# Kernel tuning notes

Hardware: AMD Instinct MI355X
Metric: run time of the kernel (lower is better)

Reference implementation:

```python
import jax, jax.numpy as jnp
import numpy as np

C_TOTAL = 201      # n_classes + 1 (background)
N_CLASSES = 200
K = 5              # n_prototypes
DIM = 768
GAMMA = 0.999
TEMPERATURE = 0.2
THRESH = 0.8       # assignment_threshold


def l2norm(x, axis=-1, eps=1e-12):
    return x / jnp.maximum(jnp.linalg.norm(x, axis=axis, keepdims=True), eps)


def setup_inputs() -> dict:
    key = jax.random.key(0)
    k0, k1, k2, k3, k4 = jax.random.split(key, 5)
    B, H, W = 32, 32, 32
    N = H * W
    patch_tokens = jax.random.normal(k0, (B, N, DIM), jnp.float32)
    raw_patch_tokens = jax.random.normal(k1, (B, N, DIM), jnp.float32)
    # trunc_normal_(std=0.02) init of the prototype buffer
    prototypes = jax.random.truncated_normal(k2, -2.0, 2.0, (C_TOTAL, K, DIM), jnp.float32) * 0.02
    sa_weights = jnp.ones((N_CLASSES, K), jnp.float32)  # constant init -> uniform softmax, same as 0.5
    labels = jax.random.randint(k3, (32,), 0, N_CLASSES)
    sam_masks = jax.random.randint(k4, (B, H, W), 0, 2, dtype=jnp.int32)
    return {
        'patch_tokens': patch_tokens,
        'raw_patch_tokens': raw_patch_tokens,
        'prototypes': prototypes,
        'sa_weights': sa_weights,
        'labels': labels,
        'sam_masks': sam_masks,
    }


def reference(patch_tokens, raw_patch_tokens, prototypes, sa_weights, labels, sam_masks):
    B, N, D = patch_tokens.shape
    H = W = int(np.sqrt(N))

    # --- prototype matching ---
    pt = l2norm(patch_tokens)
    proto_n = l2norm(prototypes)
    # [B, N, C, K] cosine logits
    logits = jnp.einsum('bnd,ckd->bnck', pt, proto_n)
    image_prototype_logits = logits.max(axis=1)                    # [B, C, K]
    saw = jax.nn.softmax(sa_weights, axis=-1) * K                  # ScoreAggregation
    class_logits = (image_prototype_logits[:, :-1, :] * saw).sum(-1) / TEMPERATURE  # [B, n_classes]

    # --- pseudo patch labels (sam_masks already at (H, W) -> nearest interp is identity) ---
    pm = sam_masks.astype(jnp.float32)                             # [B, H, W]
    pseudo = jnp.where(pm == 1.0, labels[:, None, None], N_CLASSES)  # [B, H, W] int

    # --- online clustering (vectorized over the per-class python loop) ---
    raw = l2norm(raw_patch_tokens).reshape(B * N, D)               # detached in original
    lab_flat = pseudo.reshape(-1)                                  # [BN]
    L = logits.reshape(B * N, C_TOTAL, K)
    # gather each token's logits for its own (pseudo) class: L[n, lab_flat[n], :]
    Lc = jnp.take_along_axis(L, lab_flat[:, None, None], axis=1)[:, 0, :]  # [BN, K]
    A = jax.nn.softmax(Lc, axis=-1)
    max_vals = A.max(axis=-1)
    indices = A.argmax(axis=-1)
    # threshold then L1-renormalize (zero rows stay zero, matching F.normalize eps)
    A = jnp.where(max_vals[:, None] < THRESH, 0.0, A)
    A = A / jnp.maximum(A.sum(axis=-1, keepdims=True), 1e-12)
    # per-class soft-kmeans centroid accumulation: P_c_new = A_c^T @ I_c
    wx = A[:, :, None] * raw[:, None, :]                           # [BN, K, D]
    P_c_new = jax.ops.segment_sum(wx, lab_flat, num_segments=C_TOTAL)  # [C, K, D]
    counts = jax.ops.segment_sum(jnp.ones_like(lab_flat), lab_flat, num_segments=C_TOTAL)
    present = (counts > 0)[:, None, None]
    # momentum EMA update, only for classes present in the batch
    P_new = jnp.where(present, GAMMA * prototypes + (1.0 - GAMMA) * P_c_new, prototypes)

    part_assignment_maps = (indices + lab_flat * K).reshape(B, H * W)

    return (class_logits, image_prototype_logits, logits, part_assignment_maps, P_new, pseudo)
```

## Files before the change

kernel.cpp:

```cpp
#include <hip/hip_runtime.h>
#include <math.h>

#define Bv   32
#define Nv   1024
#define Dv   768
#define Cv   201
#define Kv   5
#define CKv  1005
#define BNv  32768
#define NCLS 200

#define OFF_CL     0
#define OFF_IPL    6400
#define OFF_LOG    38560
#define OFF_PART   32970400
#define OFF_PNEW   33003168
#define OFF_PSEUDO 33775008

typedef short bf16x8 __attribute__((ext_vector_type(8)));
typedef float f32x4  __attribute__((ext_vector_type(4)));
typedef float f32x4u __attribute__((ext_vector_type(4), aligned(4)));
typedef __attribute__((address_space(1))) const unsigned int g_u32;
typedef __attribute__((address_space(3))) unsigned int l_u32;

__device__ inline unsigned short f2bf(float f) {
  unsigned u = __float_as_uint(f);
  u += 0x7fffu + ((u >> 16) & 1u);
  return (unsigned short)(u >> 16);
}
__device__ inline unsigned fenc(float f) {
  unsigned u = __float_as_uint(f);
  return u ^ (((unsigned)((int)u >> 31)) | 0x80000000u);
}
__device__ inline float fdec(unsigned u) {
  unsigned bits = (u & 0x80000000u) ? (u ^ 0x80000000u) : ~u;
  return __uint_as_float(bits);
}

__global__ __launch_bounds__(256) void prep_kernel(
    const float* __restrict__ pt, const float* __restrict__ raw,
    const float* __restrict__ proto,
    unsigned short* __restrict__ Ah, unsigned short* __restrict__ Bh,
    float* __restrict__ inv_raw, int* __restrict__ zbuf, int zn, int ZB) {
  if ((int)blockIdx.x < ZB) {
    int i = blockIdx.x * 256 + threadIdx.x;
    if (i < zn) zbuf[i] = 0;
    return;
  }
  const int rbase = (blockIdx.x - ZB) * 16 + (threadIdx.x >> 6) * 4;
  const int l = threadIdx.x & 63;

  if (rbase < BNv) {
    const float* src = pt + (size_t)rbase * Dv;
    float4 v[4][3];
#pragma unroll
    for (int r = 0; r < 4; ++r)
#pragma unroll
      for (int i = 0; i < 3; ++i)
        v[r][i] = reinterpret_cast<const float4*>(src + (size_t)r * Dv)[i * 64 + l];
    float s[4];
#pragma unroll
    for (int r = 0; r < 4; ++r)
      s[r] = v[r][0].x * v[r][0].x + v[r][0].y * v[r][0].y + v[r][0].z * v[r][0].z + v[r][0].w * v[r][0].w
           + v[r][1].x * v[r][1].x + v[r][1].y * v[r][1].y + v[r][1].z * v[r][1].z + v[r][1].w * v[r][1].w
           + v[r][2].x * v[r][2].x + v[r][2].y * v[r][2].y + v[r][2].z * v[r][2].z + v[r][2].w * v[r][2].w;
#pragma unroll
    for (int off = 32; off > 0; off >>= 1)
#pragma unroll
      for (int r = 0; r < 4; ++r) s[r] += __shfl_xor(s[r], off);
#pragma unroll
    for (int r = 0; r < 4; ++r) {
      float inv = 1.0f / fmaxf(sqrtf(s[r]), 1e-12f);
      unsigned short* dst = Ah + (size_t)(rbase + r) * Dv;
#pragma unroll
      for (int i = 0; i < 3; ++i) {
        float a0 = v[r][i].x * inv, a1 = v[r][i].y * inv;
        float a2 = v[r][i].z * inv, a3 = v[r][i].w * inv;
        *reinterpret_cast<ushort4*>(dst + i * 256 + 4 * l) =
            make_ushort4(f2bf(a0), f2bf(a1), f2bf(a2), f2bf(a3));
      }
    }
    return;
  }
  if (rbase < BNv + 1024) {
    const int rp0 = rbase - BNv;
    float4 v[4][3];
#pragma unroll
    for (int r = 0; r < 4; ++r) {
      int rp = rp0 + r;
      int rs = (rp < CKv) ? rp : (CKv - 1);
      const float* src = proto + (size_t)rs * Dv;
#pragma unroll
      for (int i = 0; i < 3; ++i)
        v[r][i] = reinterpret_cast<const float4*>(src)[i * 64 + l];
    }
    float s[4];
#pragma unroll
    for (int r = 0; r < 4; ++r)
      s[r] = v[r][0].x * v[r][0].x + v[r][0].y * v[r][0].y + v[r][0].z * v[r][0].z + v[r][0].w * v[r][0].w
           + v[r][1].x * v[r][1].x + v[r][1].y * v[r][1].y + v[r][1].z * v[r][1].z + v[r][1].w * v[r][1].w
           + v[r][2].x * v[r][2].x + v[r][2].y * v[r][2].y + v[r][2].z * v[r][2].z + v[r][2].w * v[r][2].w;
#pragma unroll
    for (int off = 32; off > 0; off >>= 1)
#pragma unroll
      for (int r = 0; r < 4; ++r) s[r] += __shfl_xor(s[r], off);
#pragma unroll
    for (int r = 0; r < 4; ++r) {
      int rp = rp0 + r;
      unsigned short* dst = Bh + (size_t)rp * Dv;
      float inv = (rp < CKv) ? 1.0f / fmaxf(sqrtf(s[r]), 1e-12f) : 0.0f;
#pragma unroll
      for (int i = 0; i < 3; ++i) {
        float a0 = v[r][i].x * inv, a1 = v[r][i].y * inv;
        float a2 = v[r][i].z * inv, a3 = v[r][i].w * inv;
        ushort4 w = (rp < CKv)
            ? make_ushort4(f2bf(a0), f2bf(a1), f2bf(a2), f2bf(a3))
            : make_ushort4(0, 0, 0, 0);
        *reinterpret_cast<ushort4*>(dst + i * 256 + 4 * l) = w;
      }
    }
    return;
  }
  if (rbase < 2 * BNv + 1024) {
    const int rr = rbase - BNv - 1024;
    const float* src = raw + (size_t)rr * Dv;
    float s[4];
#pragma unroll
    for (int r = 0; r < 4; ++r) {
      float4 v0 = reinterpret_cast<const float4*>(src + (size_t)r * Dv)[l];
      float4 v1 = reinterpret_cast<const float4*>(src + (size_t)r * Dv)[64 + l];
      float4 v2 = reinterpret_cast<const float4*>(src + (size_t)r * Dv)[128 + l];
      s[r] = v0.x * v0.x + v0.y * v0.y + v0.z * v0.z + v0.w * v0.w
           + v1.x * v1.x + v1.y * v1.y + v1.z * v1.z + v1.w * v1.w
           + v2.x * v2.x + v2.y * v2.y + v2.z * v2.z + v2.w * v2.w;
    }
#pragma unroll
    for (int off = 32; off > 0; off >>= 1)
#pragma unroll
      for (int r = 0; r < 4; ++r) s[r] += __shfl_xor(s[r], off);
    if (l == 0) {
#pragma unroll
      for (int r = 0; r < 4; ++r)
        inv_raw[rr + r] = 1.0f / fmaxf(sqrtf(s[r]), 1e-12f);
    }
  }
}

#define BM 256
#define BN 128
__global__ __launch_bounds__(512) void gemm_mfma_kernel(
    const unsigned short* __restrict__ Ah, const unsigned short* __restrict__ Bh,
    float* __restrict__ Co, unsigned int* __restrict__ iplU) {
  __shared__ __align__(16) unsigned char smem[49152];
#define LA(b) ((unsigned short (*)[32])(smem + (b) * 16384))
#define LB(b) ((unsigned short (*)[32])(smem + 32768 + (b) * 8192))
  const int tid  = threadIdx.x;
  const int wid  = tid >> 6;
  const int lane = tid & 63;
  const int wm = wid >> 1, wn = wid & 1;
  const int orig = blockIdx.x;
  const int wgid = ((orig & 7) << 7) | (orig >> 3);
  const int m0 = (wgid >> 3) * BM, n0 = (wgid & 7) * BN;
  const int fr = lane & 15;
  const int q  = lane >> 4;

  f32x4 acc[4][4];
#pragma unroll
  for (int i = 0; i < 4; ++i)
#pragma unroll
    for (int j = 0; j < 4; ++j)
#pragma unroll
      for (int r = 0; r < 4; ++r) acc[i][j][r] = 0.f;

  const int ra = wid * 16 + (lane >> 2);
  const int sa = (lane & 3) ^ ((ra >> 1) & 3);
  const unsigned short* srcA0 = Ah + (size_t)(m0 + ra) * Dv + sa * 8;
  const unsigned short* srcA1 = Ah + (size_t)(m0 + 128 + ra) * Dv + sa * 8;
  const unsigned short* srcB0 = Bh + (size_t)(n0 + ra) * Dv + sa * 8;

#define STG_A0(buf, t) __builtin_amdgcn_global_load_lds((g_u32*)(srcA0 + (t) * 32), \
    (l_u32*)&LA(buf)[wid * 16][0], 16, 0, 0)
#define STG_A1(buf, t) __builtin_amdgcn_global_load_lds((g_u32*)(srcA1 + (t) * 32), \
    (l_u32*)&LA(buf)[128 + wid * 16][0], 16, 0, 0)
#define STG_B0(buf, t) __builtin_amdgcn_global_load_lds((g_u32*)(srcB0 + (t) * 32), \
    (l_u32*)&LB(buf)[wid * 16][0], 16, 0, 0)

  const int slotR = (q ^ ((fr >> 1) & 3)) * 8;

  STG_A0(0, 0); STG_A1(0, 0); STG_B0(0, 0);

#pragma unroll 2
  for (int t = 0; t < 24; ++t) {
    const int cur = t & 1;
    if (t < 23) {
      STG_A0(cur ^ 1, t + 1); STG_A1(cur ^ 1, t + 1); STG_B0(cur ^ 1, t + 1);
      asm volatile("s_waitcnt vmcnt(3)" ::: "memory");
    } else {
      asm volatile("s_waitcnt vmcnt(0)" ::: "memory");
    }
    __builtin_amdgcn_s_barrier();
    __builtin_amdgcn_sched_barrier(0);

    bf16x8 a[4];
#pragma unroll
    for (int ph = 0; ph < 2; ++ph) {
      if (ph == 0) {
#pragma unroll
        for (int i = 0; i < 4; ++i)
          a[i] = *reinterpret_cast<const bf16x8*>(&LA(cur)[wm * 64 + i * 16 + fr][slotR]);
      }
      bf16x8 b0 = *reinterpret_cast<const bf16x8*>(&LB(cur)[wn * 64 + (ph * 2) * 16 + fr][slotR]);
      bf16x8 b1 = *reinterpret_cast<const bf16x8*>(&LB(cur)[wn * 64 + (ph * 2 + 1) * 16 + fr][slotR]);
      asm volatile("s_waitcnt lgkmcnt(0)" ::: "memory");
      __builtin_amdgcn_sched_barrier(0);
      __builtin_amdgcn_s_setprio(1);
#pragma unroll
      for (int i = 0; i < 4; ++i) {
        acc[i][ph * 2]     = __builtin_amdgcn_mfma_f32_16x16x32_bf16(a[i], b0, acc[i][ph * 2], 0, 0, 0);
        acc[i][ph * 2 + 1] = __builtin_amdgcn_mfma_f32_16x16x32_bf16(a[i], b1, acc[i][ph * 2 + 1], 0, 0, 0);
      }
      __builtin_amdgcn_s_setprio(0);
      __builtin_amdgcn_sched_barrier(0);
      __builtin_amdgcn_s_barrier();
      __builtin_amdgcn_sched_barrier(0);
    }
  }
#undef STG_A0
#undef STG_A1
#undef STG_B0

  const int b_img = m0 >> 10;
#pragma unroll
  for (int j = 0; j < 4; ++j) {
    int n = n0 + wn * 64 + j * 16 + fr;
    bool ok = (n < CKv);
    float cmax = -INFINITY;
#pragma unroll
    for (int i = 0; i < 4; ++i)
#pragma unroll
      for (int r = 0; r < 4; ++r) cmax = fmaxf(cmax, acc[i][j][r]);
    cmax = fmaxf(cmax, __shfl_xor(cmax, 16));
    cmax = fmaxf(cmax, __shfl_xor(cmax, 32));
    if (lane < 16 && ok)
      atomicMax(&iplU[(size_t)b_img * 1024 + n], fenc(cmax));
  }

  float (*ebuf)[132] = (float (*)[132])smem;
  const int r2 = lane >> 5;
  const int cl = (lane & 31) * 4;
#pragma unroll
  for (int p = 0; p < 4; ++p) {
    __syncthreads();
    if (wm == p) {
#pragma unroll
      for (int i = 0; i < 4; ++i)
#pragma unroll
        for (int j = 0; j < 4; ++j)
#pragma unroll
          for (int r = 0; r < 4; ++r)
            ebuf[i * 16 + q * 4 + r][wn * 64 + j * 16 + fr] = acc[i][j][r];
    }
    __syncthreads();
#pragma unroll
    for (int rr = 0; rr < 8; rr += 2) {
      int row = wid * 8 + rr + r2;
      f32x4 v = *reinterpret_cast<const f32x4*>(&ebuf[row][cl]);
      int gc = n0 + cl;
      size_t base = (size_t)(m0 + p * 64 + row) * CKv + gc;
      if (gc + 3 < CKv) {
        *reinterpret_cast<f32x4u*>(&Co[base]) = v;
      } else {
#pragma unroll
        for (int e = 0; e < 4; ++e)
          if (gc + e < CKv) Co[base + e] = v[e];
      }
    }
  }
#undef LA
#undef LB
}

__global__ __launch_bounds__(256) void accum_fused_kernel(
    const float* __restrict__ logits, const int* __restrict__ labels,
    const int* __restrict__ sam, const float* __restrict__ raw,
    const float* __restrict__ inv_raw, float* __restrict__ out,
    float* __restrict__ P_acc, int* __restrict__ present,
    const unsigned int* __restrict__ iplU, const float* __restrict__ sa_w) {
  const int b = blockIdx.x;
  const int y = blockIdx.y;
  const int z = blockIdx.z;
  if (z == 8) {
    if (y != 0) return;
    int c = threadIdx.x;
    if (c >= Cv) return;
    float r[Kv];
#pragma unroll
    for (int k = 0; k < Kv; ++k) {
      r[k] = fdec(iplU[(size_t)b * 1024 + c * Kv + k]);
      out[OFF_IPL + (size_t)(b * Cv + c) * Kv + k] = r[k];
    }
    if (c < NCLS) {
      float w[Kv], wm = -INFINITY;
#pragma unroll
      for (int k = 0; k < Kv; ++k) { w[k] = sa_w[c * Kv + k]; wm = fmaxf(wm, w[k]); }
      float es = 0.f;
#pragma unroll
      for (int k = 0; k < Kv; ++k) { w[k] = expf(w[k] - wm); es += w[k]; }
      float cl = 0.f;
#pragma unroll
      for (int k = 0; k < Kv; ++k) cl += r[k] * (w[k] / es * (float)Kv);
      out[OFF_CL + b * NCLS + c] = cl / 0.2f;
    }
    return;
  }

  __shared__ float As[128][Kv];
  __shared__ float Sc[128];
  __shared__ int   Ls[128];
  const int t0 = z * 128;
  if (threadIdx.x < 128) {
    int n = b * Nv + t0 + threadIdx.x;
    int lab = (sam[n] == 1) ? labels[b] : NCLS;
    const float* p = logits + (size_t)n * CKv + lab * Kv;
    float L[Kv];
#pragma unroll
    for (int k = 0; k < Kv; ++k) L[k] = p[k];
    float mv = L[0];
    int idx = 0;
#pragma unroll
    for (int k = 1; k < Kv; ++k)
      if (L[k] > mv) { mv = L[k]; idx = k; }
    float e[Kv], s = 0.f;
#pragma unroll
    for (int k = 0; k < Kv; ++k) { e[k] = expf(L[k] - mv); s += e[k]; }
    float inv = 1.0f / s;
    float scale = (inv < 0.8f) ? 0.f : inv;
#pragma unroll
    for (int k = 0; k < Kv; ++k) As[threadIdx.x][k] = e[k] * scale;
    Ls[threadIdx.x] = lab;
    Sc[threadIdx.x] = inv_raw[n];
    if (y == 0) {
      out[OFF_PSEUDO + n] = (float)lab;
      out[OFF_PART + n] = (float)(idx + lab * Kv);
      present[lab] = 1;
    }
  }
  __syncthreads();

  const int d = y * 256 + threadIdx.x;
  float accL[Kv] = {}, accB[Kv] = {};
#pragma unroll 4
  for (int t = 0; t < 128; ++t) {
    int n2 = b * Nv + t0 + t;
    float rv = raw[(size_t)n2 * Dv + d] * Sc[t];
    if (Ls[t] == NCLS) {
#pragma unroll
      for (int k = 0; k < Kv; ++k) accB[k] = fmaf(As[t][k], rv, accB[k]);
    } else {
#pragma unroll
      for (int k = 0; k < Kv; ++k) accL[k] = fmaf(As[t][k], rv, accL[k]);
    }
  }
  int lab = labels[b];
#pragma unroll
  for (int k = 0; k < Kv; ++k) atomicAdd(&P_acc[((size_t)lab * Kv + k) * Dv + d], accL[k]);
#pragma unroll
  for (int k = 0; k < Kv; ++k) atomicAdd(&P_acc[((size_t)NCLS * Kv + k) * Dv + d], accB[k]);
}

__global__ __launch_bounds__(256) void pnew_kernel(
    const float* __restrict__ proto, const float* __restrict__ P_acc,
    const int* __restrict__ present, float* __restrict__ out) {
  int i = blockIdx.x * 256 + threadIdx.x;
  if (i >= Cv * Kv * Dv) return;
  int c = i / (Kv * Dv);
  float p = proto[i];
  out[OFF_PNEW + i] = present[c] ? 0.999f * p + 0.001f * P_acc[i] : p;
}

extern "C" void kernel_launch(void* const* d_in, const int* in_sizes, int n_in,
                              void* d_out, int out_size, void* d_ws, size_t ws_size,
                              hipStream_t stream) {
  const float* pt     = (const float*)d_in[0];
  const float* raw    = (const float*)d_in[1];
  const float* proto  = (const float*)d_in[2];
  const float* sa_w   = (const float*)d_in[3];
  const int*   labels = (const int*)d_in[4];
  const int*   sam    = (const int*)d_in[5];
  float* out = (float*)d_out;

  float* A_buf   = (float*)d_ws;
  int*   tok_lab = (int*)(A_buf + (size_t)BNv * Kv);
  float* P_acc   = (float*)(tok_lab + BNv);
  int*   present = (int*)(P_acc + (size_t)Cv * Kv * Dv);
  unsigned int* iplU = (unsigned int*)(present + 256);
  float* inv_raw = (float*)(iplU + BNv);
  unsigned short* Ah = (unsigned short*)(inv_raw + BNv);
  unsigned short* Bh = Ah + (size_t)BNv * Dv;

  int nz = Cv * Kv * Dv + 256 + BNv;
  int ZB = (nz + 255) / 256;
  int prep_rows_blocks = (2 * BNv + 1024) / 16;

  prep_kernel<<<ZB + prep_rows_blocks, 256, 0, stream>>>(
      pt, raw, proto, Ah, Bh, inv_raw, (int*)P_acc, nz, ZB);

  gemm_mfma_kernel<<<(BNv / BM) * (1024 / BN), 512, 0, stream>>>(
      Ah, Bh, out + OFF_LOG, iplU);

  accum_fused_kernel<<<dim3(Bv, Dv / 256, 9), 256, 0, stream>>>(
      out + OFF_LOG, labels, sam, raw, inv_raw, out, P_acc, present, iplU, sa_w);

  pnew_kernel<<<(Cv * Kv * Dv + 255) / 256, 256, 0, stream>>>(
      proto, P_acc, present, out);
}
```

Before: 183.6 us.

## Move raw-token norm computation into extra GEMM blocks to overlap with matmul

The inverse L2 norms of raw_patch_tokens are no longer computed by prep_kernel. 256 extra blocks are appended to the GEMM launch, and each computes norms for 128 rows. The aim is to run this memory-bound reduction alongside the compute-bound MFMA GEMM so it no longer adds serially to prep time. The risk is that the extra blocks compete for CUs and HBM bandwidth with the GEMM tiles, and the 512-thread blocks with their large LDS allocation may schedule less densely.

```diff
diff --git a/kernel.cpp b/kernel.cpp
--- a/kernel.cpp
+++ b/kernel.cpp
@@ -38,10 +38,9 @@
 }
 
 __global__ __launch_bounds__(256) void prep_kernel(
-    const float* __restrict__ pt, const float* __restrict__ raw,
-    const float* __restrict__ proto,
+    const float* __restrict__ pt, const float* __restrict__ proto,
     unsigned short* __restrict__ Ah, unsigned short* __restrict__ Bh,
-    float* __restrict__ inv_raw, int* __restrict__ zbuf, int zn, int ZB) {
+    int* __restrict__ zbuf, int zn, int ZB) {
   if ((int)blockIdx.x < ZB) {
     int i = blockIdx.x * 256 + threadIdx.x;
     if (i < zn) zbuf[i] = 0;
@@ -121,35 +120,13 @@
     }
     return;
   }
-  if (rbase < 2 * BNv + 1024) {
-    const int rr = rbase - BNv - 1024;
-    const float* src = raw + (size_t)rr * Dv;
-    float s[4];
-#pragma unroll
-    for (int r = 0; r < 4; ++r) {
-      float4 v0 = reinterpret_cast<const float4*>(src + (size_t)r * Dv)[l];
-      float4 v1 = reinterpret_cast<const float4*>(src + (size_t)r * Dv)[64 + l];
-      float4 v2 = reinterpret_cast<const float4*>(src + (size_t)r * Dv)[128 + l];
-      s[r] = v0.x * v0.x + v0.y * v0.y + v0.z * v0.z + v0.w * v0.w
-           + v1.x * v1.x + v1.y * v1.y + v1.z * v1.z + v1.w * v1.w
-           + v2.x * v2.x + v2.y * v2.y + v2.z * v2.z + v2.w * v2.w;
-    }
-#pragma unroll
-    for (int off = 32; off > 0; off >>= 1)
-#pragma unroll
-      for (int r = 0; r < 4; ++r) s[r] += __shfl_xor(s[r], off);
-    if (l == 0) {
-#pragma unroll
-      for (int r = 0; r < 4; ++r)
-        inv_raw[rr + r] = 1.0f / fmaxf(sqrtf(s[r]), 1e-12f);
-    }
-  }
 }
 
 #define BM 256
 #define BN 128
 __global__ __launch_bounds__(512) void gemm_mfma_kernel(
     const unsigned short* __restrict__ Ah, const unsigned short* __restrict__ Bh,
+    const float* __restrict__ raw, float* __restrict__ inv_raw,
     float* __restrict__ Co, unsigned int* __restrict__ iplU) {
   __shared__ __align__(16) unsigned char smem[49152];
 #define LA(b) ((unsigned short (*)[32])(smem + (b) * 16384))
@@ -157,8 +134,40 @@
   const int tid  = threadIdx.x;
   const int wid  = tid >> 6;
   const int lane = tid & 63;
+  const int orig = blockIdx.x;
+
+  if (orig >= 1024) {
+    const int base_row = (orig - 1024) * 128 + wid * 16;
+    for (int it = 0; it < 16; it += 2) {
+      const float* s0p = raw + (size_t)(base_row + it) * Dv;
+      const float* s1p = s0p + Dv;
+      float4 v[2][3];
+#pragma unroll
+      for (int i = 0; i < 3; ++i)
+        v[0][i] = reinterpret_cast<const float4*>(s0p)[i * 64 + lane];
+#pragma unroll
+      for (int i = 0; i < 3; ++i)
+        v[1][i] = reinterpret_cast<const float4*>(s1p)[i * 64 + lane];
+      float s[2];
+#pragma unroll
+      for (int r = 0; r < 2; ++r)
+        s[r] = v[r][0].x * v[r][0].x + v[r][0].y * v[r][0].y + v[r][0].z * v[r][0].z + v[r][0].w * v[r][0].w
+             + v[r][1].x * v[r][1].x + v[r][1].y * v[r][1].y + v[r][1].z * v[r][1].z + v[r][1].w * v[r][1].w
+             + v[r][2].x * v[r][2].x + v[r][2].y * v[r][2].y + v[r][2].z * v[r][2].z + v[r][2].w * v[r][2].w;
+#pragma unroll
+      for (int off = 32; off > 0; off >>= 1) {
+        s[0] += __shfl_xor(s[0], off);
+        s[1] += __shfl_xor(s[1], off);
+      }
+      if (lane == 0) {
+        inv_raw[base_row + it]     = 1.0f / fmaxf(sqrtf(s[0]), 1e-12f);
+        inv_raw[base_row + it + 1] = 1.0f / fmaxf(sqrtf(s[1]), 1e-12f);
+      }
+    }
+    return;
+  }
+
   const int wm = wid >> 1, wn = wid & 1;
-  const int orig = blockIdx.x;
   const int wgid = ((orig & 7) << 7) | (orig >> 3);
   const int m0 = (wgid >> 3) * BM, n0 = (wgid & 7) * BN;
   const int fr = lane & 15;
@@ -400,13 +409,13 @@
 
   int nz = Cv * Kv * Dv + 256 + BNv;
   int ZB = (nz + 255) / 256;
-  int prep_rows_blocks = (2 * BNv + 1024) / 16;
+  int prep_rows_blocks = (BNv + 1024) / 16;
 
   prep_kernel<<<ZB + prep_rows_blocks, 256, 0, stream>>>(
-      pt, raw, proto, Ah, Bh, inv_raw, (int*)P_acc, nz, ZB);
-
-  gemm_mfma_kernel<<<(BNv / BM) * (1024 / BN), 512, 0, stream>>>(
-      Ah, Bh, out + OFF_LOG, iplU);
+      pt, proto, Ah, Bh, (int*)P_acc, nz, ZB);
+
+  gemm_mfma_kernel<<<1024 + 256, 512, 0, stream>>>(
+      Ah, Bh, raw, inv_raw, out + OFF_LOG, iplU);
 
   accum_fused_kernel<<<dim3(Bv, Dv / 256, 9), 256, 0, stream>>>(
       out + OFF_LOG, labels, sam, raw, inv_raw, out, P_acc, present, iplU, sa_w);
```

After: 176.2 us, median of 2. 1.04x faster.
